# Kernel tuning notes

Hardware: AMD Instinct MI355X
Metric: run time of the kernel (lower is better)

The kernel has to match this reference:

```python
import jax, jax.numpy as jnp
import numpy as np

R = 262144  # 512x512 rays
B = 32      # scene boxes
BIG = 1e10
EPS = 1e-4


def setup_inputs() -> dict:
    key = jax.random.key(0)
    k1, k2, k3, k4 = jax.random.split(key, 4)
    # camera-like ray origins (near a single viewpoint) and unit directions
    rays_o = jax.random.normal(k1, (R, 3), dtype=jnp.float32) * 0.1
    rays_d = jax.random.normal(k2, (R, 3), dtype=jnp.float32)
    rays_d = rays_d / jnp.linalg.norm(rays_d, axis=-1, keepdims=True)
    # axis-aligned boxes: [center_xyz, size_xyz]
    centers = jax.random.uniform(k3, (B, 3), dtype=jnp.float32, minval=-5.0, maxval=5.0)
    sizes = jax.random.uniform(k4, (B, 3), dtype=jnp.float32, minval=0.5, maxval=2.5)
    bbox = jnp.concatenate([centers, sizes], axis=1)
    return {"rays_o": rays_o, "rays_d": rays_d, "bbox": bbox}


def reference(rays_o, rays_d, bbox):
    # rays_d[rays_d == 0] = 1e-8
    rays_d = jnp.where(rays_d == 0.0, 1e-8, rays_d)
    ro = rays_o[:, None, :]  # [R,1,3]
    rd = rays_d[:, None, :]  # [R,1,3]
    bbox_min = bbox[:, :3] - bbox[:, 3:] / 2  # [B,3]
    bbox_max = bbox[:, :3] + bbox[:, 3:] / 2  # [B,3]
    # slab test: per-axis entry/exit parameters, [R,B,3]
    t_mins = (bbox_min - ro) / rd
    t_maxs = (bbox_max - ro) / rd
    t_entry = jnp.minimum(t_mins, t_maxs)  # ts.min(-1)
    t_exit = jnp.maximum(t_mins, t_maxs)   # ts.max(-1)
    t_mins_max = t_entry.max(-1)  # [R,B]
    t_maxs_min = t_exit.min(-1)   # [R,B]
    is_intersects = (t_mins_max < t_maxs_min) & (t_maxs_min > 0)
    keep = is_intersects.any(-1)  # [R]
    # candidate hit points at each per-axis entry t: [R,B,3(axis),3(xyz)]
    t_nears = t_entry
    pts = ro[:, :, None, :] + t_nears[..., None] * rd[:, :, None, :]
    valid = ((pts >= (bbox_min[None, :, None, :] - EPS)) &
             (pts <= (bbox_max[None, :, None, :] + EPS))).all(-1)
    valid = valid & (t_nears >= 0)
    t_nears = jnp.where(valid, t_nears, BIG)
    t_near = t_nears.min(-1)  # [R,B]
    # argsort(...)[:, 0] == argmin over boxes
    first_min = jnp.argmin(t_near, axis=-1)  # [R]
    nearest_bbox_idx = jnp.where(keep, first_min, -1).astype(jnp.int64)
    nearest_distance_2d = jnp.where(
        keep, jnp.take_along_axis(t_near, first_min[:, None], axis=1)[:, 0], -1.0)
    return nearest_bbox_idx, nearest_distance_2d
```

## Files before the change

### kernel.cpp

```cpp
#include <hip/hip_runtime.h>


typedef float v2f __attribute__((ext_vector_type(2)));

constexpr int BMAX = 32;
constexpr int HALF = BMAX / 2;

__device__ __forceinline__ v2f pk_add(v2f a, v2f b) {
    v2f d;
    asm("v_pk_add_f32 %0, %1, %2" : "=v"(d) : "v"(a), "v"(b));
    return d;
}
__device__ __forceinline__ v2f pk_mul(v2f a, v2f b) {
    v2f d;
    asm("v_pk_mul_f32 %0, %1, %2" : "=v"(d) : "v"(a), "v"(b));
    return d;
}
__device__ __forceinline__ v2f pk_fma(v2f a, v2f b, v2f c) {
    v2f d;
    asm("v_pk_fma_f32 %0, %1, %2, %3" : "=v"(d) : "v"(a), "v"(b), "v"(c));
    return d;
}

__global__ __launch_bounds__(256) void ray_aabb_kernel(
    const float* __restrict__ rays_o,
    const float* __restrict__ rays_d,
    const float* __restrict__ bbox,
    float* __restrict__ out_idx,
    float* __restrict__ out_dist,
    int R)
{
    const float BIG = 10000000000.0f;
    const float EPS = 1e-4f;

    __shared__ float4 s_q[BMAX][3];

    int t = threadIdx.x;
    if (t < BMAX) {
        int b = t;
        int slot = (b & 15) * 2 + (b >> 4);
        float lo[3], hi[3], loE[3], hiE[3];
        #pragma unroll
        for (int a = 0; a < 3; ++a) {
            float c = bbox[b * 6 + a];
            float s = bbox[b * 6 + 3 + a];
            float h  = __fmul_rn(s, 0.5f);
            lo[a]  = __fsub_rn(c, h);
            hi[a]  = __fadd_rn(c, h);
            loE[a] = __fsub_rn(lo[a], EPS);
            hiE[a] = __fadd_rn(hi[a], EPS);
        }
        s_q[slot][0] = make_float4(lo[0], hi[0], lo[1], hi[1]);
        s_q[slot][1] = make_float4(lo[2], hi[2], loE[0], loE[1]);
        s_q[slot][2] = make_float4(loE[2], hiE[0], hiE[1], hiE[2]);
    }
    __syncthreads();

    int gid  = blockIdx.x * blockDim.x + threadIdx.x;
    int ray  = gid >> 1;
    int par  = gid & 1;
    if (ray >= R) return;
    int b0   = par * HALF;

    float ro[3], rd[3], y[3];
    v2f y2[3], nro2[3], nrd2[3];
    #pragma unroll
    for (int a = 0; a < 3; ++a) {
        ro[a] = rays_o[ray * 3 + a];
        float d = rays_d[ray * 3 + a];
        rd[a] = (d == 0.0f) ? 1e-8f : d;
        y[a]  = __fdiv_rn(1.0f, rd[a]);
        y2[a]   = v2f{y[a], y[a]};
        nro2[a] = v2f{-ro[a], -ro[a]};
        nrd2[a] = v2f{-rd[a], -rd[a]};
    }

    bool  keep  = false;
    float best  = BIG;
    int   bestb = b0;

    #pragma unroll 4
    for (int bi = 0; bi < HALF; ++bi) {
        int slot = bi * 2 + par;
        int b    = b0 + bi;
        float4 q0 = s_q[slot][0];
        float4 q1 = s_q[slot][1];
        float4 q2 = s_q[slot][2];
        v2f bnd[3];
        bnd[0] = v2f{q0.x, q0.y};
        bnd[1] = v2f{q0.z, q0.w};
        bnd[2] = v2f{q1.x, q1.y};
        float loE[3] = {q1.z, q1.w, q2.x};
        float hiE[3] = {q2.y, q2.z, q2.w};

        float entry[3], exitv[3];
        #pragma unroll
        for (int a = 0; a < 3; ++a) {
            v2f d2  = pk_add(bnd[a], nro2[a]);
            v2f q0v = pk_mul(d2, y2[a]);
            v2f e   = pk_fma(nrd2[a], q0v, d2);
            v2f qv  = pk_fma(e, y2[a], q0v);
            entry[a] = fminf(qv.x, qv.y);
            exitv[a] = fmaxf(qv.x, qv.y);
        }
        float tmm = fmaxf(entry[0], fmaxf(entry[1], entry[2]));
        float tmx = fminf(exitv[0], fminf(exitv[1], exitv[2]));
        keep = keep || ((tmm < tmx) && (tmx > 0.0f));

        bool inb[3][3];
        #pragma unroll
        for (int a = 0; a < 3; ++a) {
            int o1 = (a == 0) ? 1 : 0;
            int o2 = (a == 2) ? 1 : 2;
            float m1 = __fmul_rn(entry[o1], rd[a]);
            float m2 = __fmul_rn(entry[o2], rd[a]);
            float p1 = __fadd_rn(ro[a], m1);
            float p2 = __fadd_rn(ro[a], m2);
            inb[a][o1] = (__builtin_amdgcn_fmed3f(p1, loE[a], hiE[a]) == p1);
            inb[a][o2] = (__builtin_amdgcn_fmed3f(p2, loE[a], hiE[a]) == p2);
        }
        float tn = BIG;
        #pragma unroll
        for (int cnd = 0; cnd < 3; ++cnd) {
            int a1 = (cnd == 0) ? 1 : 0;
            int a2 = (cnd == 2) ? 1 : 2;
            bool v = (entry[cnd] >= 0.0f) && inb[a1][cnd] && inb[a2][cnd];
            if (v) tn = fminf(tn, entry[cnd]);
        }
        if (tn < best) { best = tn; bestb = b; }
    }

    float o_best  = __shfl_xor(best, 1, 64);
    int   o_bestb = __shfl_xor(bestb, 1, 64);
    int   o_keep  = __shfl_xor((int)keep, 1, 64);

    if (par == 0) {
        bool k = keep || (o_keep != 0);
        float fb = best; int fi = bestb;
        if (o_best < fb) { fb = o_best; fi = o_bestb; }
        out_idx[ray]  = k ? (float)fi : -1.0f;
        out_dist[ray] = k ? fb : -1.0f;
    }
}

extern "C" void kernel_launch(void* const* d_in, const int* in_sizes, int n_in,
                              void* d_out, int out_size, void* d_ws, size_t ws_size,
                              hipStream_t stream) {
    const float* rays_o = (const float*)d_in[0];
    const float* rays_d = (const float*)d_in[1];
    const float* bbox   = (const float*)d_in[2];
    int R = in_sizes[0] / 3;

    float* out = (float*)d_out;
    float* out_idx  = out;
    float* out_dist = out + R;

    const int threads = 256;
    const long long total = 2LL * R;
    const int blocks = (int)((total + threads - 1) / threads);
    ray_aabb_kernel<<<blocks, threads, 0, stream>>>(rays_o, rays_d, bbox,
                                                    out_idx, out_dist, R);
}
```

Before: 22.48 us.

## Replace packed-FP32 inline asm with scalar Markstein division and branchless min

Removes the v_pk_add/mul/fma inline-asm helpers and computes each slab t with scalar sub and Markstein-corrected division. The unroll of the box loop goes from 4 to 8, and the candidate-t selection becomes three selects feeding a min3 instead of a chain of conditional mins. The aim is to let the compiler schedule freely, since inline asm blocks its scheduling, and to cut the conditional chain. The cost is roughly twice as many VALU ops for the slab math, because packed instructions are no longer used, plus higher register pressure from the deeper unroll.

```diff
diff --git a/kernel.cpp b/kernel.cpp
--- a/kernel.cpp
+++ b/kernel.cpp
@@ -1,25 +1,13 @@
 #include <hip/hip_runtime.h>
 
-
-typedef float v2f __attribute__((ext_vector_type(2)));
 
 constexpr int BMAX = 32;
 constexpr int HALF = BMAX / 2;
 
-__device__ __forceinline__ v2f pk_add(v2f a, v2f b) {
-    v2f d;
-    asm("v_pk_add_f32 %0, %1, %2" : "=v"(d) : "v"(a), "v"(b));
-    return d;
-}
-__device__ __forceinline__ v2f pk_mul(v2f a, v2f b) {
-    v2f d;
-    asm("v_pk_mul_f32 %0, %1, %2" : "=v"(d) : "v"(a), "v"(b));
-    return d;
-}
-__device__ __forceinline__ v2f pk_fma(v2f a, v2f b, v2f c) {
-    v2f d;
-    asm("v_pk_fma_f32 %0, %1, %2, %3" : "=v"(d) : "v"(a), "v"(b), "v"(c));
-    return d;
+__device__ __forceinline__ float div_markstein(float a, float b, float y) {
+    float q0 = __fmul_rn(a, y);
+    float e  = __fmaf_rn(-b, q0, a);
+    return __fmaf_rn(e, y, q0);
 }
 
 __global__ __launch_bounds__(256) void ray_aabb_kernel(
@@ -63,45 +51,37 @@
     int b0   = par * HALF;
 
     float ro[3], rd[3], y[3];
-    v2f y2[3], nro2[3], nrd2[3];
     #pragma unroll
     for (int a = 0; a < 3; ++a) {
         ro[a] = rays_o[ray * 3 + a];
         float d = rays_d[ray * 3 + a];
         rd[a] = (d == 0.0f) ? 1e-8f : d;
         y[a]  = __fdiv_rn(1.0f, rd[a]);
-        y2[a]   = v2f{y[a], y[a]};
-        nro2[a] = v2f{-ro[a], -ro[a]};
-        nrd2[a] = v2f{-rd[a], -rd[a]};
     }
 
     bool  keep  = false;
     float best  = BIG;
     int   bestb = b0;
 
-    #pragma unroll 4
+    #pragma unroll 8
     for (int bi = 0; bi < HALF; ++bi) {
         int slot = bi * 2 + par;
         int b    = b0 + bi;
         float4 q0 = s_q[slot][0];
         float4 q1 = s_q[slot][1];
         float4 q2 = s_q[slot][2];
-        v2f bnd[3];
-        bnd[0] = v2f{q0.x, q0.y};
-        bnd[1] = v2f{q0.z, q0.w};
-        bnd[2] = v2f{q1.x, q1.y};
+        float lo[3]  = {q0.x, q0.z, q1.x};
+        float hi[3]  = {q0.y, q0.w, q1.y};
         float loE[3] = {q1.z, q1.w, q2.x};
         float hiE[3] = {q2.y, q2.z, q2.w};
 
         float entry[3], exitv[3];
         #pragma unroll
         for (int a = 0; a < 3; ++a) {
-            v2f d2  = pk_add(bnd[a], nro2[a]);
-            v2f q0v = pk_mul(d2, y2[a]);
-            v2f e   = pk_fma(nrd2[a], q0v, d2);
-            v2f qv  = pk_fma(e, y2[a], q0v);
-            entry[a] = fminf(qv.x, qv.y);
-            exitv[a] = fmaxf(qv.x, qv.y);
+            float t1 = div_markstein(__fsub_rn(lo[a], ro[a]), rd[a], y[a]);
+            float t2 = div_markstein(__fsub_rn(hi[a], ro[a]), rd[a], y[a]);
+            entry[a] = fminf(t1, t2);
+            exitv[a] = fmaxf(t1, t2);
         }
         float tmm = fmaxf(entry[0], fmaxf(entry[1], entry[2]));
         float tmx = fminf(exitv[0], fminf(exitv[1], exitv[2]));
@@ -119,14 +99,15 @@
             inb[a][o1] = (__builtin_amdgcn_fmed3f(p1, loE[a], hiE[a]) == p1);
             inb[a][o2] = (__builtin_amdgcn_fmed3f(p2, loE[a], hiE[a]) == p2);
         }
-        float tn = BIG;
+        float tsel[3];
         #pragma unroll
         for (int cnd = 0; cnd < 3; ++cnd) {
             int a1 = (cnd == 0) ? 1 : 0;
             int a2 = (cnd == 2) ? 1 : 2;
             bool v = (entry[cnd] >= 0.0f) && inb[a1][cnd] && inb[a2][cnd];
-            if (v) tn = fminf(tn, entry[cnd]);
+            tsel[cnd] = v ? entry[cnd] : BIG;
         }
+        float tn = fminf(tsel[0], fminf(tsel[1], tsel[2]));
         if (tn < best) { best = tn; bestb = b; }
     }
 
```

Result: faster. 20.73 us (median of 2 runs) (-7.8%).
